# Performance work log

Hardware: AMD Instinct MI355X
Metric: run time of the kernel (lower is better)

The kernel has to match this reference:

```python
import jax, jax.numpy as jnp
import numpy as np

H = 16      # num_heads
HD = 128    # head_dim = embed_dim // num_heads
BS = 64     # NSA block_size
SEL = 8     # selected blocks per query (block_counts)
WIN = 64    # sliding window (left) size
BASE = 10000.0


def _rope(t):
    # t: [b, n, h, hd]; rotary LRPE (lrpe_type=1)
    n, hd = t.shape[1], t.shape[-1]
    half = hd // 2
    inv = 1.0 / (BASE ** (jnp.arange(half, dtype=jnp.float32) / half))
    th = jnp.arange(n, dtype=jnp.float32)[:, None] * inv[None, :]  # [n, half]
    cos = jnp.cos(th)[None, :, None, :]
    sin = jnp.sin(th)[None, :, None, :]
    t1, t2 = t[..., :half], t[..., half:]
    return jnp.concatenate([t1 * cos - t2 * sin, t1 * sin + t2 * cos], axis=-1)


def _nsa_forward(x, Wq, Wk, Wv, Wg, Wo):
    b, n, d = x.shape
    nb = n // BS
    scale = HD ** -0.5
    q = (x @ Wq).reshape(b, n, H, HD)
    k = (x @ Wk).reshape(b, n, H, HD)
    v = (x @ Wv).reshape(b, n, H, HD)
    g = jax.nn.sigmoid(x @ Wg)                   # [b, n, 3H]
    g_cmp, g_slc, g_swa = jnp.split(g, 3, axis=-1)
    q = _rope(q)
    k = _rope(k)
    idx = jnp.arange(n)

    # --- compression branch: mean-pooled KV blocks, causal over fully-past blocks
    k_cmp = k.reshape(b, nb, BS, H, HD).mean(axis=2)   # [b, nb, h, hd]
    v_cmp = v.reshape(b, nb, BS, H, HD).mean(axis=2)
    s_cmp = jnp.einsum('bnhd,bmhd->bhnm', q, k_cmp) * scale  # [b, h, n, nb]
    blk_end = (jnp.arange(nb) + 1) * BS - 1
    cmp_mask = idx[:, None] >= blk_end[None, :]        # [n, nb]
    p_cmp = jax.nn.softmax(jnp.where(cmp_mask[None, None], s_cmp, -1e30), axis=-1)
    p_cmp = p_cmp * cmp_mask.any(-1)[None, None, :, None]  # zero rows with no valid block
    o_cmp = jnp.einsum('bhnm,bmhd->bnhd', p_cmp, v_cmp)

    # --- selection branch: top-k blocks by compressed scores, current block forced
    cur_blk = jax.nn.one_hot(idx // BS, nb, dtype=jnp.float32)  # [n, nb]
    imp = p_cmp + 2.0 * cur_blk[None, None]
    sel = jax.lax.top_k(imp, SEL)[1]                   # [b, h, n, SEL]
    blk_sel = jax.nn.one_hot(sel, nb).sum(-2) > 0      # [b, h, n, nb]
    causal = idx[:, None] >= idx[None, :]              # [n, n]
    slc_mask = blk_sel[..., idx // BS] & causal[None, None]  # [b, h, n, n]
    s_full = jnp.einsum('bnhd,bmhd->bhnm', q, k) * scale     # [b, h, n, n]
    p_slc = jax.nn.softmax(jnp.where(slc_mask, s_full, -1e30), axis=-1)
    o_slc = jnp.einsum('bhnm,bmhd->bnhd', p_slc, v)

    swa_mask = causal & (idx[:, None] - idx[None, :] <= WIN)
    p_swa = jax.nn.softmax(jnp.where(swa_mask[None, None], s_full, -1e30), axis=-1)
    o_swa = jnp.einsum('bhnm,bmhd->bnhd', p_swa, v)

    o = (o_cmp * g_cmp[..., None] + o_slc * g_slc[..., None]
         + o_swa * g_swa[..., None])                   # [b, n, h, hd]
    return o.reshape(b, n, H * HD) @ Wo


def setup_inputs() -> dict:
    key = jax.random.key(0)
    ks = jax.random.split(key, 6)
    B, N, D = 2, 1024, 2048
    std = 0.02
    return {
        'x': jax.random.normal(ks[0], (B, N, D), jnp.float32),
        'Wq': jax.random.normal(ks[1], (D, H * HD), jnp.float32) * std,
        'Wk': jax.random.normal(ks[2], (D, H * HD), jnp.float32) * std,
        'Wv': jax.random.normal(ks[3], (D, H * HD), jnp.float32) * std,
        'Wg': jax.random.normal(ks[4], (D, 3 * H), jnp.float32) * std,
        'Wo': jax.random.normal(ks[5], (H * HD, D), jnp.float32) * std,
    }


def reference(x, Wq, Wk, Wv, Wg, Wo):
    return _nsa_forward(x, Wq, Wk, Wv, Wg, Wo)
```

## Files before the change

kernel.cpp:

```cpp
#include <hip/hip_runtime.h>
#include <hip/hip_bf16.h>

#define HN   16
#define HDIM 128
#define NSEQ 1024
#define NBLK 16
#define BSZ  64
#define SCALE 0.08838834764831845f
#define QKV_STR 6400
#define KOFS 2048
#define VOFS 4096
#define GOFS 6144

typedef __attribute__((ext_vector_type(8))) short bfrag;
typedef __attribute__((ext_vector_type(4))) float facc;

__device__ __forceinline__ float bf2f(short s) {
  union { unsigned u; float f; } cv;
  cv.u = ((unsigned)(unsigned short)s) << 16;
  return cv.f;
}
__device__ __forceinline__ short f2bf(float f) {
  unsigned u = __float_as_uint(f);
  u = (u + 0x7fff + ((u >> 16) & 1)) >> 16;
  return (short)u;
}

#define ASYNC16(gp, lp)                                                    \
  __builtin_amdgcn_global_load_lds(                                        \
      (const __attribute__((address_space(1))) void*)(gp),                 \
      (__attribute__((address_space(3))) void*)(lp), 16, 0, 0)

#define MFMA16(a, b, c) __builtin_amdgcn_mfma_f32_16x16x32_bf16(a, b, c, 0, 0, 0)

__global__ __launch_bounds__(256) void prep(const float* __restrict__ Wq,
                                            const float* __restrict__ Wk,
                                            const float* __restrict__ Wv,
                                            const float* __restrict__ Wg,
                                            const float* __restrict__ Wo,
                                            const float* __restrict__ x,
                                            short* __restrict__ w_t,
                                            short* __restrict__ wo_t,
                                            short* __restrict__ x_bf,
                                            float2* __restrict__ tbl) {
  __shared__ float tile[32][33];
  const int z = blockIdx.z;
  const int bx = blockIdx.x * 32, by = blockIdx.y * 32;
  const int tx = threadIdx.x & 31, ty = threadIdx.x >> 5;
  if (z == 5) {
    if (blockIdx.y >= 4) return;
    int i = (blockIdx.y * 64 + blockIdx.x) * 256 + threadIdx.x;
    int d = i & 63, n = i >> 6;
    float inv = expf(-(float)d * (9.210340371976184f / 64.0f));
    float sn, cs;
    sincosf((float)n * inv, &sn, &cs);
    tbl[i] = make_float2(cs, sn);
    return;
  }
  if (z == 4) {
#pragma unroll
    for (int i = 0; i < 4; ++i) {
      const int row = by + ty + 8 * i;
      x_bf[(size_t)row * 2048 + bx + tx] = f2bf(x[(size_t)row * 2048 + bx + tx]);
    }
    return;
  }
  if (z == 3) {
    if (blockIdx.x >= 4) return;
#pragma unroll
    for (int i = 0; i < 4; ++i) {
      const int c = bx + tx;
      tile[ty + 8 * i][tx] = (c < 48) ? Wg[(size_t)(by + ty + 8 * i) * 48 + c] : 0.f;
    }
    __syncthreads();
#pragma unroll
    for (int i = 0; i < 4; ++i)
      w_t[(size_t)(GOFS + bx + ty + 8 * i) * 2048 + by + tx] = f2bf(tile[tx][ty + 8 * i]);
    return;
  }
  if (z == 6) {
#pragma unroll
    for (int i = 0; i < 4; ++i)
      tile[ty + 8 * i][tx] = Wo[(size_t)(by + ty + 8 * i) * 2048 + bx + tx];
    __syncthreads();
#pragma unroll
    for (int i = 0; i < 4; ++i)
      wo_t[(size_t)(bx + ty + 8 * i) * 2048 + by + tx] = f2bf(tile[tx][ty + 8 * i]);
    return;
  }
  const float* src = (z == 0) ? Wq : (z == 1) ? Wk : Wv;
#pragma unroll
  for (int i = 0; i < 4; ++i)
    tile[ty + 8 * i][tx] = src[(size_t)(by + ty + 8 * i) * 2048 + bx + tx];
  __syncthreads();
#pragma unroll
  for (int i = 0; i < 4; ++i)
    w_t[(size_t)(z * 2048 + bx + ty + 8 * i) * 2048 + by + tx] = f2bf(tile[tx][ty + 8 * i]);
}

__global__ __launch_bounds__(512, 1) void gemm256(const short* __restrict__ A,
                                                  const short* __restrict__ Bt,
                                                  short* __restrict__ C,
                                                  int M, int N, int K) {
  __shared__ short lds[2][2][16384];
  const int t = threadIdx.x;
  const int l = t & 63, w = t >> 6;
  const int wm = w >> 2, wn = w & 3;
  const int lm = l & 15, hi = l >> 4;
  const int lanexor = (lm & 7) << 3;
  const int kk0 = (hi * 8) ^ lanexor;
  const int L = blockIdx.x;
  const int item = (L & 7) * (gridDim.x >> 3) + (L >> 3);
  const int nrow = M >> 8;
  const int row0 = (item % nrow) * 256, col0 = (item / nrow) * 256;
  const int nt = K >> 6;
  const int ni = nt >> 1;

  const int srow = t >> 3;
  const int scol = 8 * ((t & 7) ^ (srow & 7));
  const short* Ab = A + (size_t)(row0 + srow) * K + scol;
  const short* Bb = Bt + (size_t)(col0 + srow) * K + scol;

#define STAGE(mat, srcbase, h, tau, buf)                                     \
  {                                                                          \
    const short* g_ = (srcbase) + (size_t)(h) * 128 * K + (size_t)(tau) * 64;\
    short* d_ = &lds[buf][mat][(h) * 8192 + t * 8];                          \
    ASYNC16(g_, d_);                                                         \
    ASYNC16(g_ + (size_t)64 * K, d_ + 4096);                                 \
  }

#define DS_A(qm, cb)                                                         \
  _Pragma("unroll") for (int ii = 0; ii < 4; ++ii) {                         \
    const int row_ = wm * 128 + (qm) * 64 + ii * 16 + lm;                    \
    af[ii * 2 + 0] = *(const bfrag*)&lds[cb][0][row_ * 64 + kk0];            \
    af[ii * 2 + 1] = *(const bfrag*)&lds[cb][0][row_ * 64 + (kk0 ^ 32)];     \
  }
#define DS_B(qn, arr, cb)                                                    \
  _Pragma("unroll") for (int jj = 0; jj < 2; ++jj) {                         \
    const int row_ = wn * 64 + (qn) * 32 + jj * 16 + lm;                     \
    arr[jj * 2 + 0] = *(const bfrag*)&lds[cb][1][row_ * 64 + kk0];           \
    arr[jj * 2 + 1] = *(const bfrag*)&lds[cb][1][row_ * 64 + (kk0 ^ 32)];    \
  }
#define QUAD(qm, qn, arr)                                                    \
  _Pragma("unroll") for (int ii = 0; ii < 4; ++ii)                           \
  _Pragma("unroll") for (int jj = 0; jj < 2; ++jj) {                         \
    acc[(qm)*4+ii][(qn)*2+jj] = MFMA16(af[ii*2+0], arr[jj*2+0], acc[(qm)*4+ii][(qn)*2+jj]); \
    acc[(qm)*4+ii][(qn)*2+jj] = MFMA16(af[ii*2+1], arr[jj*2+1], acc[(qm)*4+ii][(qn)*2+jj]); \
  }
#define BARLG                                                                \
  __builtin_amdgcn_s_barrier();                                              \
  asm volatile("s_waitcnt lgkmcnt(0)" ::: "memory");                         \
  __builtin_amdgcn_sched_barrier(0)
#define PRIO1 __builtin_amdgcn_s_setprio(1)
#define PRIO0 __builtin_amdgcn_s_setprio(0)
#define BAR __builtin_amdgcn_s_barrier()

  facc acc[8][4] = {};
  bfrag af[8], bf0[4], bf1[4];

  STAGE(0, Ab, 0, 0, 0); STAGE(0, Ab, 1, 0, 0);
  STAGE(1, Bb, 0, 0, 0); STAGE(1, Bb, 1, 0, 0);
  STAGE(1, Bb, 0, 1, 1); STAGE(1, Bb, 1, 1, 1);
  asm volatile("s_waitcnt vmcnt(4)" ::: "memory");
  BAR;

  for (int i = 0; i < ni; ++i) {
    const int t1 = 2 * i + 1;
    const int g2 = (2 * i + 2 < nt) ? 2 * i + 2 : 2 * i;
    const int g3 = (2 * i + 3 < nt) ? 2 * i + 3 : t1;

    DS_A(0, 0); DS_B(0, bf0, 0);
    STAGE(0, Ab, 0, t1, 1);
    BARLG; PRIO1; QUAD(0, 0, bf0); PRIO0; BAR;

    DS_B(1, bf1, 0);
    STAGE(0, Ab, 1, t1, 1);
    BARLG; PRIO1; QUAD(0, 1, bf1); PRIO0; BAR;

    DS_A(1, 0);
    STAGE(1, Bb, 0, g2, 0);
    BARLG; PRIO1; QUAD(1, 1, bf1); PRIO0; BAR;

    STAGE(1, Bb, 1, g2, 0);
    PRIO1; QUAD(1, 0, bf0); PRIO0;
    asm volatile("s_waitcnt vmcnt(4)" ::: "memory");
    BAR;

    DS_A(0, 1); DS_B(0, bf0, 1);
    STAGE(0, Ab, 0, g2, 0);
    BARLG; PRIO1; QUAD(0, 0, bf0); PRIO0; BAR;

    DS_B(1, bf1, 1);
    STAGE(0, Ab, 1, g2, 0);
    BARLG; PRIO1; QUAD(0, 1, bf1); PRIO0; BAR;

    DS_A(1, 1);
    STAGE(1, Bb, 0, g3, 1);
    BARLG; PRIO1; QUAD(1, 1, bf1); PRIO0; BAR;

    STAGE(1, Bb, 1, g3, 1);
    PRIO1; QUAD(1, 0, bf0); PRIO0;
    asm volatile("s_waitcnt vmcnt(4)" ::: "memory");
    BAR;
  }

#pragma unroll
  for (int i = 0; i < 8; ++i)
#pragma unroll
    for (int j = 0; j < 4; ++j)
#pragma unroll
      for (int rr = 0; rr < 4; ++rr)
        C[(size_t)(row0 + wm * 128 + i * 16 + hi * 4 + rr) * N +
          col0 + wn * 64 + j * 16 + lm] = f2bf(acc[i][j][rr]);
#undef STAGE
#undef DS_A
#undef DS_B
#undef QUAD
#undef BARLG
#undef PRIO1
#undef PRIO0
#undef BAR
}

__device__ __forceinline__ void store_c(float* p, float v) { *p = v; }
__device__ __forceinline__ void store_c(short* p, float v) { *p = f2bf(v); }

template <typename OT>
__global__ __launch_bounds__(512, 1) void gemm_bf16_bt(const short* __restrict__ A,
                                                       const short* __restrict__ Bt,
                                                       OT* __restrict__ C,
                                                       int M, int N, int K) {
  __shared__ short As[128 * 32];
  __shared__ short Bs[128 * 32];
  const int t = threadIdx.x;
  const int l = t & 63, w = t >> 6;
  const int wr = w >> 2, wc = w & 3;
  const int lm = l & 15, lk = (l >> 4) * 8;
  const int L = blockIdx.x;
  const int xcd = L & 7, j = L >> 3;
  const int rowt = (xcd & 3) * 4 + (j & 3);
  const int colt = (xcd >> 2) * 8 + (j >> 2);
  const int row0 = rowt * 128, col0 = colt * 128;
  facc acc[4][2] = {};

  const int sr = t >> 2;
  const int sk = (t & 3) * 8;
  const short* Ag = A + (size_t)(row0 + sr) * K + sk;
  const short* Bg = Bt + (size_t)(col0 + sr) * K + sk;
  short* la = As + t * 8;
  short* lb = Bs + t * 8;

  for (int k0 = 0; k0 < K; k0 += 32) {
    ASYNC16(Ag + k0, la);
    ASYNC16(Bg + k0, lb);
    __syncthreads();
    bfrag af[4], bf[2];
#pragma unroll
    for (int i = 0; i < 4; ++i)
      af[i] = *(const bfrag*)&As[(wr * 64 + i * 16 + lm) * 32 + lk];
#pragma unroll
    for (int j2 = 0; j2 < 2; ++j2)
      bf[j2] = *(const bfrag*)&Bs[(wc * 32 + j2 * 16 + lm) * 32 + lk];
#pragma unroll
    for (int i = 0; i < 4; ++i)
#pragma unroll
      for (int j2 = 0; j2 < 2; ++j2)
        acc[i][j2] = MFMA16(af[i], bf[j2], acc[i][j2]);
    __syncthreads();
  }

  const int orow = row0 + wr * 64 + (l >> 4) * 4;
  const int ocol = col0 + wc * 32 + lm;
#pragma unroll
  for (int i = 0; i < 4; ++i)
#pragma unroll
    for (int j2 = 0; j2 < 2; ++j2)
#pragma unroll
      for (int rr = 0; rr < 4; ++rr)
        store_c(&C[(size_t)(orow + i * 16 + rr) * N + ocol + j2 * 16], acc[i][j2][rr]);
}

__global__ __launch_bounds__(256) void postqkv(short* __restrict__ qkv,
                                               const float2* __restrict__ tbl,
                                               float* __restrict__ kc,
                                               short* __restrict__ vt,
                                               short* __restrict__ vct) {
  const int nb = blockIdx.x, h = blockIdx.y, b = blockIdx.z;
  const int t = threadIdx.x;
  const int n0 = nb * 64;
  __shared__ short tile[64][136];

  const int row = t >> 2;
  const int c16 = (t & 3) * 16;
  const float2* tp = tbl + (size_t)(n0 + row) * 64 + c16;

#pragma unroll
  for (int qk = 0; qk < 2; ++qk) {
    short* base = qkv + (size_t)(b * NSEQ + n0 + row) * QKV_STR + qk * KOFS + h * HDIM + c16;
    bfrag lo0 = *(const bfrag*)base;
    bfrag lo1 = *(const bfrag*)(base + 8);
    bfrag hi0 = *(const bfrag*)(base + 64);
    bfrag hi1 = *(const bfrag*)(base + 72);
    bfrag olo0, olo1, ohi0, ohi1;
#pragma unroll
    for (int j = 0; j < 8; ++j) {
      float2 cs0 = tp[j], cs1 = tp[j + 8];
      float a0 = bf2f(lo0[j]), b0 = bf2f(hi0[j]);
      float a1 = bf2f(lo1[j]), b1 = bf2f(hi1[j]);
      olo0[j] = f2bf(a0 * cs0.x - b0 * cs0.y);
      ohi0[j] = f2bf(a0 * cs0.y + b0 * cs0.x);
      olo1[j] = f2bf(a1 * cs1.x - b1 * cs1.y);
      ohi1[j] = f2bf(a1 * cs1.y + b1 * cs1.x);
    }
    *(bfrag*)base = olo0;
    *(bfrag*)(base + 8) = olo1;
    *(bfrag*)(base + 64) = ohi0;
    *(bfrag*)(base + 72) = ohi1;
    if (qk == 1) {
      *(bfrag*)&tile[row][c16] = olo0;
      *(bfrag*)&tile[row][c16 + 8] = olo1;
      *(bfrag*)&tile[row][c16 + 64] = ohi0;
      *(bfrag*)&tile[row][c16 + 72] = ohi1;
    }
  }
  __syncthreads();

  if (t < 128) {
    float s = 0.f;
#pragma unroll 8
    for (int r = 0; r < 64; ++r) s += bf2f(tile[r][t]);
    kc[(((size_t)(b * NBLK + nb) * HN) + h) * 128 + t] = s * (1.0f / 64.0f);
  }
  __syncthreads();

#pragma unroll
  for (int it = 0; it < 4; ++it) {
    int idx = t + 256 * it;
    int r2 = idx >> 4, ch = idx & 15;
    *(bfrag*)&tile[r2][ch * 8] =
        *(const bfrag*)&qkv[(size_t)(b * NSEQ + n0 + r2) * QKV_STR + VOFS + h * HDIM + ch * 8];
  }
  __syncthreads();

#pragma unroll
  for (int it = 0; it < 4; ++it) {
    int idx = t + 256 * it;
    int d = idx >> 3, ch = idx & 7;
    bfrag tv;
    float s = 0.f;
#pragma unroll
    for (int j = 0; j < 8; ++j) {
      tv[j] = tile[ch * 8 + j][d];
      s += bf2f(tv[j]);
    }
    *(bfrag*)&vt[(((size_t)(b * HN + h) * 128) + d) * 1024 + n0 + ch * 8] = tv;
    s += __shfl_down(s, 4);
    s += __shfl_down(s, 2);
    s += __shfl_down(s, 1);
    if ((t & 7) == 0)
      vct[(((size_t)(b * HN + h) * 128) + d) * 16 + nb] = f2bf(s * (1.0f / 64.0f));
  }
}

__global__ __launch_bounds__(64) void cmp_sel(const short* __restrict__ qkv,
                                              const float* __restrict__ kc,
                                              short* __restrict__ pc,
                                              int* __restrict__ sel) {
  int i = blockIdx.x * 64 + threadIdx.x;
  int n = i & 1023;
  int h = (i >> 10) & 15;
  int b = i >> 14;
  const short* qp = qkv + (size_t)(b * NSEQ + n) * QKV_STR + h * HDIM;
  const int nv = (n + 1) >> 6;
  float s[NBLK];
#pragma unroll
  for (int m = 0; m < NBLK; ++m) s[m] = 0.f;
  for (int d0 = 0; d0 < HDIM; d0 += 8) {
    bfrag qv = *(const bfrag*)&qp[d0];
    float qf[8];
#pragma unroll
    for (int dd = 0; dd < 8; ++dd) qf[dd] = bf2f(qv[dd]);
    for (int m = 0; m < nv; ++m) {
      const float4* kp = (const float4*)(kc + ((size_t)((b * NBLK + m) * HN + h) << 7) + d0);
      const float4 k0 = kp[0], k1 = kp[1];
      s[m] += qf[0] * k0.x + qf[1] * k0.y + qf[2] * k0.z + qf[3] * k0.w +
              qf[4] * k1.x + qf[5] * k1.y + qf[6] * k1.z + qf[7] * k1.w;
    }
  }
  float mx = -1e30f;
  for (int m = 0; m < nv; ++m) { s[m] *= SCALE; mx = fmaxf(mx, s[m]); }
  float den = 0.f;
  for (int m = 0; m < nv; ++m) { s[m] = __expf(s[m] - mx); den += s[m]; }
  const float rden = (nv > 0) ? 1.0f / den : 0.f;
  float p[NBLK];
#pragma unroll
  for (int m = 0; m < NBLK; ++m) p[m] = (m < nv) ? s[m] * rden : 0.f;
  bfrag o0, o1;
#pragma unroll
  for (int m = 0; m < 8; ++m) { o0[m] = f2bf(p[m]); o1[m] = f2bf(p[m + 8]); }
  bfrag* pout = (bfrag*)(pc + (size_t)i * 16);
  pout[0] = o0; pout[1] = o1;
  p[n >> 6] += 2.0f;
  int mask = 0;
#pragma unroll
  for (int ss = 0; ss < 8; ++ss) {
    int best = 0;
    float bv = -1e30f;
#pragma unroll
    for (int m = 0; m < NBLK; ++m)
      if (p[m] > bv) { bv = p[m]; best = m; }
    mask |= 1 << best;
    p[best] = -1e30f;
  }
  sel[i] = mask;
}

__global__ __launch_bounds__(512, 1) void attn_mfma(
    const short* __restrict__ qkv, const short* __restrict__ vt,
    const short* __restrict__ vct, const short* __restrict__ pc,
    const int* __restrict__ sel, short* __restrict__ o) {
  const int fid = blockIdx.x;
  const int xcd = fid & 7;
  const int idx = fid >> 3;
  const int pair = (xcd << 2) | (idx & 3);
  const int rblk = idx >> 2;
  const int h = pair & 15, b = pair >> 4;

  const int tid = threadIdx.x;
  const int wid = tid >> 6;
  const int l = tid & 63;
  const int lm = l & 15, hi = l >> 4;
  const int rt = wid * 8 + rblk;
  const int nbase = rt * 16;
  const int CTMAX = ((56 + rblk) * 16) >> 6;

  __shared__ short kbuf[3][8192];
  __shared__ short vbuf[3][8192];
  __shared__ short pbuf[8][2][1024];
  short* p_slc = &pbuf[wid][0][0];
  short* p_swa = &pbuf[wid][1][0];

  const short* qrow = qkv + (size_t)(b * NSEQ + nbase + lm) * QKV_STR + h * HDIM;
  bfrag qf[4];
#pragma unroll
  for (int ks = 0; ks < 4; ++ks) qf[ks] = *(const bfrag*)&qrow[32 * ks + 8 * hi];

  int selrow = sel[(size_t)(b * HN + h) * NSEQ + nbase + lm];
  int uni = selrow;
#pragma unroll
  for (int m = 1; m < 16; m <<= 1) uni |= __shfl_xor(uni, m);
  int sel4[4];
#pragma unroll
  for (int rg = 0; rg < 4; ++rg) sel4[rg] = __shfl(selrow, 4 * hi + rg);

  const int thi = nbase >> 6;
  const int tlo = (nbase >= 64) ? ((nbase - 64) >> 6) : 0;
  const int wmask = (int)((2u << thi) - (1u << tlo));
  const unsigned am = (unsigned)(uni | wmask) & (unsigned)((2u << thi) - 1);

  facc acc_slc[8] = {}, acc_swa[8] = {};
  float ps_s[4] = {0.f, 0.f, 0.f, 0.f}, ps_w[4] = {0.f, 0.f, 0.f, 0.f};

#define STAGEKV(ct_, buf_)                                                   \
  {                                                                          \
    _Pragma("unroll") for (int rr = 0; rr < 2; ++rr) {                       \
      const int i2 = tid + 512 * rr;                                         \
      const int rw = i2 >> 4, cc = i2 & 15;                                  \
      const short* g_ = qkv + (size_t)(b * NSEQ + (ct_) * 64 + rw) * QKV_STR \
                        + KOFS + h * HDIM + 8 * (cc ^ (rw & 7));             \
      ASYNC16(g_, &kbuf[buf_][i2 * 8]);                                      \
    }                                                                        \
    _Pragma("unroll") for (int rr = 0; rr < 2; ++rr) {                       \
      const int i2 = tid + 512 * rr;                                         \
      const int dd = i2 >> 3, cc = i2 & 7;                                   \
      const short* g_ = vt + ((size_t)(b * HN + h) * 128 + dd) * 1024        \
                        + (ct_) * 64 + 8 * (cc ^ (dd & 7));                  \
      ASYNC16(g_, &vbuf[buf_][i2 * 8]);                                      \
    }                                                                        \
  }

#define EXPF(f_)                                                            \
  _Pragma("unroll") for (int rg = 0; rg < 4; ++rg) {                        \
    const int col_ = ct * 64 + 16 * (f_) + lm;                              \
    const int row_ = nbase + 4 * hi + rg;                                   \
    float e_ = __expf(sacc[f_][rg] * SCALE);                                \
    e_ = (col_ <= row_) ? e_ : 0.f;                                         \
    float es_ = ((sel4[rg] >> ct) & 1) ? e_ : 0.f;                          \
    float ew_ = (row_ - col_ <= 64) ? e_ : 0.f;                             \
    ps_s[rg] += es_;                                                        \
    ps_w[rg] += ew_;                                                        \
    const int srow_ = 4 * hi + rg;                                          \
    const int sidx_ = (64 * srow_ + 16 * (f_) + lm) ^ ((srow_ & 7) << 3);   \
    if (do_s) p_slc[sidx_] = f2bf(es_);                                     \
    if (do_w) p_swa[sidx_] = f2bf(ew_);                                     \
  }

  STAGEKV(0, 0);
  STAGEKV(1, 1);
  asm volatile("s_waitcnt vmcnt(4)" ::: "memory");
  __syncthreads();

  int cur = 0;
  for (int ct = 0; ct <= CTMAX; ++ct) {
    const bool have_next2 = (ct + 2 <= CTMAX);
    if (have_next2) {
      const int nb2 = (cur + 2 >= 3) ? cur - 1 : cur + 2;
      const int ct2 = ct + 2;
      STAGEKV(ct2, nb2);
    }

    if ((am >> ct) & 1) {
      const bool do_s = (uni >> ct) & 1;
      const bool do_w = (wmask >> ct) & 1;

      facc sacc[4] = {};
#pragma unroll
      for (int f = 0; f < 4; ++f) {
        const int row_ = 16 * f + lm;
        const int rx = row_ & 7;
        bfrag k0 = *(const bfrag*)&kbuf[cur][row_ * 128 + 8 * ((0 + hi) ^ rx)];
        bfrag k1 = *(const bfrag*)&kbuf[cur][row_ * 128 + 8 * ((4 + hi) ^ rx)];
        bfrag k2 = *(const bfrag*)&kbuf[cur][row_ * 128 + 8 * ((8 + hi) ^ rx)];
        bfrag k3 = *(const bfrag*)&kbuf[cur][row_ * 128 + 8 * ((12 + hi) ^ rx)];
        sacc[f] = MFMA16(qf[0], k0, sacc[f]);
        sacc[f] = MFMA16(qf[1], k1, sacc[f]);
        sacc[f] = MFMA16(qf[2], k2, sacc[f]);
        sacc[f] = MFMA16(qf[3], k3, sacc[f]);
      }

      EXPF(0); EXPF(1); EXPF(2); EXPF(3);

#pragma unroll
      for (int ks = 0; ks < 2; ++ks) {
        const int ridx = (64 * lm + 8 * hi + 32 * ks) ^ ((lm & 7) << 3);
        bfrag pas = {}, paw = {};
        if (do_s) pas = *(const bfrag*)&p_slc[ridx];
        if (do_w) paw = *(const bfrag*)&p_swa[ridx];
#pragma unroll
        for (int df = 0; df < 8; ++df) {
          const int d_ = 16 * df + lm;
          bfrag vb = *(const bfrag*)&vbuf[cur][d_ * 64 + 8 * ((4 * ks + hi) ^ (d_ & 7))];
          if (do_s) acc_slc[df] = MFMA16(pas, vb, acc_slc[df]);
          if (do_w) acc_swa[df] = MFMA16(paw, vb, acc_swa[df]);
        }
      }
    }

    if (ct < CTMAX) {
      if (have_next2)
        asm volatile("s_waitcnt vmcnt(4)" ::: "memory");
      else
        asm volatile("s_waitcnt vmcnt(0)" ::: "memory");
      __syncthreads();
    }
    cur = (cur + 1 >= 3) ? 0 : cur + 1;
  }
#undef STAGEKV
#undef EXPF

  facc acc_cmp[8] = {};
  {
    bfrag pa = {};
    if (hi < 2)
      pa = *(const bfrag*)&pc[((size_t)(b * HN + h) * NSEQ + nbase + lm) * 16 + 8 * hi];
#pragma unroll
    for (int df = 0; df < 8; ++df) {
      bfrag vb = {};
      if (hi < 2)
        vb = *(const bfrag*)&vct[(((size_t)(b * HN + h) * 128) + 16 * df + lm) * 16 + 8 * hi];
      acc_cmp[df] = MFMA16(pa, vb, acc_cmp[df]);
    }
  }

#pragma unroll
  for (int m = 1; m < 16; m <<= 1) {
#pragma unroll
    for (int rg = 0; rg < 4; ++rg) {
      ps_s[rg] += __shfl_xor(ps_s[rg], m);
      ps_w[rg] += __shfl_xor(ps_w[rg], m);
    }
  }

  float inv_s[4], inv_w[4], gcv[4], gsv[4], gwv[4];
#pragma unroll
  for (int rg = 0; rg < 4; ++rg) {
    inv_s[rg] = 1.0f / ps_s[rg];
    inv_w[rg] = 1.0f / ps_w[rg];
    const short* gp = qkv + (size_t)(b * NSEQ + nbase + 4 * hi + rg) * QKV_STR + GOFS;
    gcv[rg] = 1.0f / (1.0f + __expf(-bf2f(gp[h])));
    gsv[rg] = 1.0f / (1.0f + __expf(-bf2f(gp[16 + h])));
    gwv[rg] = 1.0f / (1.0f + __expf(-bf2f(gp[32 + h])));
  }

  short* obase = o + (size_t)(b * NSEQ + nbase) * 2048 + h * HDIM;
#pragma unroll
  for (int df = 0; df < 8; ++df)
#pragma unroll
    for (int rg = 0; rg < 4; ++rg) {
      float val = gcv[rg] * acc_cmp[df][rg] +
                  gsv[rg] * acc_slc[df][rg] * inv_s[rg] +
                  gwv[rg] * acc_swa[df][rg] * inv_w[rg];
      obase[(size_t)(4 * hi + rg) * 2048 + 16 * df + lm] = f2bf(val);
    }
}

extern "C" void kernel_launch(void* const* d_in, const int* in_sizes, int n_in,
                              void* d_out, int out_size, void* d_ws, size_t ws_size,
                              hipStream_t stream) {
  const float* x  = (const float*)d_in[0];
  const float* Wq = (const float*)d_in[1];
  const float* Wk = (const float*)d_in[2];
  const float* Wv = (const float*)d_in[3];
  const float* Wg = (const float*)d_in[4];
  const float* Wo = (const float*)d_in[5];
  float* out = (float*)d_out;

  char* w = (char*)d_ws;
  short* x_bf = (short*)w;
  short* o_bf = x_bf;
  w += (size_t)2048 * 2048 * 2;
  short* w_t  = (short*)w;
  w += (size_t)6400 * 2048 * 2;
  short* qkv  = (short*)w;
  w += (size_t)2048 * 6400 * 2;
  float* kc   = (float*)w; w += (size_t)65536 * 4;
  short* vct  = (short*)w; w += (size_t)65536 * 2;
  short* pcb  = (short*)w; w += (size_t)524288 * 2;
  int*   sel  = (int*)w;   w += (size_t)32768 * 4;
  short* vt   = (short*)w; w += (size_t)4194304 * 2;
  float2* tbl = (float2*)w; w += (size_t)65536 * 8;
  short* wo_t = (short*)w; w += (size_t)2048 * 2048 * 2;

  const dim3 blk(256);
  prep<<<dim3(64, 64, 7), blk, 0, stream>>>(Wq, Wk, Wv, Wg, Wo, x, w_t, wo_t, x_bf, tbl);
  gemm256<<<200, dim3(512), 0, stream>>>(x_bf, w_t, qkv, 2048, 6400, 2048);
  postqkv<<<dim3(16, 16, 2), blk, 0, stream>>>(qkv, tbl, kc, vt, vct);
  cmp_sel<<<512, dim3(64), 0, stream>>>(qkv, kc, pcb, sel);
  attn_mfma<<<256, dim3(512), 0, stream>>>(qkv, vt, vct, pcb, sel, o_bf);
  gemm_bf16_bt<float><<<256, dim3(512), 0, stream>>>(o_bf, wo_t, out, 2048, 2048, 2048);
}
```

Baseline: 226.5 us.

## Replace 256x256 QKV GEMM with 128x128 tiled kernel over 800 blocks

The fused QKV+gate projection GEMM moves from a 256x256 tile with 512 threads and a 4-phase double-buffered schedule to a 128x128 tile with 256 threads and a simpler per-k-step double buffer. The grid grows from 200 to 800 workgroups, which fills the device's compute units more evenly instead of leaving some idle with 200 large tiles. In exchange, per-tile data reuse is halved, so more global and LDS traffic is needed, and the pipeline waits on vmcnt(0) every step, which exposes load latency.

```diff
diff --git a/kernel.cpp b/kernel.cpp
--- a/kernel.cpp
+++ b/kernel.cpp
@@ -98,128 +98,100 @@
     w_t[(size_t)(z * 2048 + bx + ty + 8 * i) * 2048 + by + tx] = f2bf(tile[tx][ty + 8 * i]);
 }
 
-__global__ __launch_bounds__(512, 1) void gemm256(const short* __restrict__ A,
+__global__ __launch_bounds__(256, 1) void gemm128(const short* __restrict__ A,
                                                   const short* __restrict__ Bt,
                                                   short* __restrict__ C,
                                                   int M, int N, int K) {
-  __shared__ short lds[2][2][16384];
+  __shared__ short lds[2][2][8192];
   const int t = threadIdx.x;
   const int l = t & 63, w = t >> 6;
-  const int wm = w >> 2, wn = w & 3;
+  const int wr = w >> 1, wc = w & 1;
   const int lm = l & 15, hi = l >> 4;
-  const int lanexor = (lm & 7) << 3;
-  const int kk0 = (hi * 8) ^ lanexor;
+  const int r7 = lm & 7;
+  const int kk0 = 8 * (hi ^ r7);
   const int L = blockIdx.x;
   const int item = (L & 7) * (gridDim.x >> 3) + (L >> 3);
-  const int nrow = M >> 8;
-  const int row0 = (item % nrow) * 256, col0 = (item / nrow) * 256;
+  const int nrow = M >> 7;
+  const int row0 = (item % nrow) * 128, col0 = (item / nrow) * 128;
   const int nt = K >> 6;
-  const int ni = nt >> 1;
-
-  const int srow = t >> 3;
-  const int scol = 8 * ((t & 7) ^ (srow & 7));
-  const short* Ab = A + (size_t)(row0 + srow) * K + scol;
-  const short* Bb = Bt + (size_t)(col0 + srow) * K + scol;
-
-#define STAGE(mat, srcbase, h, tau, buf)                                     \
-  {                                                                          \
-    const short* g_ = (srcbase) + (size_t)(h) * 128 * K + (size_t)(tau) * 64;\
-    short* d_ = &lds[buf][mat][(h) * 8192 + t * 8];                          \
-    ASYNC16(g_, d_);                                                         \
-    ASYNC16(g_ + (size_t)64 * K, d_ + 4096);                                 \
-  }
-
-#define DS_A(qm, cb)                                                         \
+
+  const short* Ab = A + (size_t)row0 * K;
+  const short* Bb = Bt + (size_t)col0 * K;
+
+#define STG(mat, base, tau, buf)                                             \
+  _Pragma("unroll") for (int j2 = 0; j2 < 4; ++j2) {                         \
+    const int idx2 = t + 256 * j2;                                           \
+    const int rw = idx2 >> 3, cc = idx2 & 7;                                 \
+    ASYNC16((base) + (size_t)rw * K + (size_t)(tau) * 64 + 8 * (cc ^ (rw & 7)), \
+            &lds[buf][mat][idx2 * 8]);                                       \
+  }
+#define DS_A(cb)                                                             \
   _Pragma("unroll") for (int ii = 0; ii < 4; ++ii) {                         \
-    const int row_ = wm * 128 + (qm) * 64 + ii * 16 + lm;                    \
+    const int row_ = wr * 64 + ii * 16 + lm;                                 \
     af[ii * 2 + 0] = *(const bfrag*)&lds[cb][0][row_ * 64 + kk0];            \
     af[ii * 2 + 1] = *(const bfrag*)&lds[cb][0][row_ * 64 + (kk0 ^ 32)];     \
   }
-#define DS_B(qn, arr, cb)                                                    \
+#define DS_B(q, arr, cb)                                                     \
   _Pragma("unroll") for (int jj = 0; jj < 2; ++jj) {                         \
-    const int row_ = wn * 64 + (qn) * 32 + jj * 16 + lm;                     \
+    const int row_ = wc * 64 + (q) * 32 + jj * 16 + lm;                      \
     arr[jj * 2 + 0] = *(const bfrag*)&lds[cb][1][row_ * 64 + kk0];           \
     arr[jj * 2 + 1] = *(const bfrag*)&lds[cb][1][row_ * 64 + (kk0 ^ 32)];    \
   }
-#define QUAD(qm, qn, arr)                                                    \
+#define HALF(q, arr)                                                         \
   _Pragma("unroll") for (int ii = 0; ii < 4; ++ii)                           \
   _Pragma("unroll") for (int jj = 0; jj < 2; ++jj) {                         \
-    acc[(qm)*4+ii][(qn)*2+jj] = MFMA16(af[ii*2+0], arr[jj*2+0], acc[(qm)*4+ii][(qn)*2+jj]); \
-    acc[(qm)*4+ii][(qn)*2+jj] = MFMA16(af[ii*2+1], arr[jj*2+1], acc[(qm)*4+ii][(qn)*2+jj]); \
+    acc[ii][(q)*2+jj] = MFMA16(af[ii*2+0], arr[jj*2+0], acc[ii][(q)*2+jj]);  \
+    acc[ii][(q)*2+jj] = MFMA16(af[ii*2+1], arr[jj*2+1], acc[ii][(q)*2+jj]);  \
   }
 #define BARLG                                                                \
   __builtin_amdgcn_s_barrier();                                              \
   asm volatile("s_waitcnt lgkmcnt(0)" ::: "memory");                         \
   __builtin_amdgcn_sched_barrier(0)
-#define PRIO1 __builtin_amdgcn_s_setprio(1)
-#define PRIO0 __builtin_amdgcn_s_setprio(0)
-#define BAR __builtin_amdgcn_s_barrier()
-
-  facc acc[8][4] = {};
+
+  facc acc[4][4] = {};
   bfrag af[8], bf0[4], bf1[4];
 
-  STAGE(0, Ab, 0, 0, 0); STAGE(0, Ab, 1, 0, 0);
-  STAGE(1, Bb, 0, 0, 0); STAGE(1, Bb, 1, 0, 0);
-  STAGE(1, Bb, 0, 1, 1); STAGE(1, Bb, 1, 1, 1);
-  asm volatile("s_waitcnt vmcnt(4)" ::: "memory");
-  BAR;
-
-  for (int i = 0; i < ni; ++i) {
-    const int t1 = 2 * i + 1;
-    const int g2 = (2 * i + 2 < nt) ? 2 * i + 2 : 2 * i;
-    const int g3 = (2 * i + 3 < nt) ? 2 * i + 3 : t1;
-
-    DS_A(0, 0); DS_B(0, bf0, 0);
-    STAGE(0, Ab, 0, t1, 1);
-    BARLG; PRIO1; QUAD(0, 0, bf0); PRIO0; BAR;
-
-    DS_B(1, bf1, 0);
-    STAGE(0, Ab, 1, t1, 1);
-    BARLG; PRIO1; QUAD(0, 1, bf1); PRIO0; BAR;
-
-    DS_A(1, 0);
-    STAGE(1, Bb, 0, g2, 0);
-    BARLG; PRIO1; QUAD(1, 1, bf1); PRIO0; BAR;
-
-    STAGE(1, Bb, 1, g2, 0);
-    PRIO1; QUAD(1, 0, bf0); PRIO0;
-    asm volatile("s_waitcnt vmcnt(4)" ::: "memory");
-    BAR;
-
-    DS_A(0, 1); DS_B(0, bf0, 1);
-    STAGE(0, Ab, 0, g2, 0);
-    BARLG; PRIO1; QUAD(0, 0, bf0); PRIO0; BAR;
-
-    DS_B(1, bf1, 1);
-    STAGE(0, Ab, 1, g2, 0);
-    BARLG; PRIO1; QUAD(0, 1, bf1); PRIO0; BAR;
-
-    DS_A(1, 1);
-    STAGE(1, Bb, 0, g3, 1);
-    BARLG; PRIO1; QUAD(1, 1, bf1); PRIO0; BAR;
-
-    STAGE(1, Bb, 1, g3, 1);
-    PRIO1; QUAD(1, 0, bf0); PRIO0;
-    asm volatile("s_waitcnt vmcnt(4)" ::: "memory");
-    BAR;
-  }
-
-#pragma unroll
-  for (int i = 0; i < 8; ++i)
+  STG(0, Ab, 0, 0);
+  STG(1, Bb, 0, 0);
+  asm volatile("s_waitcnt vmcnt(0)" ::: "memory");
+  __builtin_amdgcn_s_barrier();
+
+  for (int tau = 0; tau < nt; ++tau) {
+    const int c = tau & 1;
+    const int tn = (tau + 1 < nt) ? tau + 1 : tau;
+
+    DS_A(c); DS_B(0, bf0, c);
+    STG(0, Ab, tn, c ^ 1);
+    BARLG;
+    __builtin_amdgcn_s_setprio(1);
+    HALF(0, bf0);
+    __builtin_amdgcn_s_setprio(0);
+    __builtin_amdgcn_s_barrier();
+
+    DS_B(1, bf1, c);
+    STG(1, Bb, tn, c ^ 1);
+    BARLG;
+    __builtin_amdgcn_s_setprio(1);
+    HALF(1, bf1);
+    __builtin_amdgcn_s_setprio(0);
+    asm volatile("s_waitcnt vmcnt(0)" ::: "memory");
+    __builtin_amdgcn_s_barrier();
+  }
+
+  const int orow = row0 + wr * 64 + hi * 4;
+  const int ocol = col0 + wc * 64 + lm;
+#pragma unroll
+  for (int i = 0; i < 4; ++i)
 #pragma unroll
     for (int j = 0; j < 4; ++j)
 #pragma unroll
       for (int rr = 0; rr < 4; ++rr)
-        C[(size_t)(row0 + wm * 128 + i * 16 + hi * 4 + rr) * N +
-          col0 + wn * 64 + j * 16 + lm] = f2bf(acc[i][j][rr]);
-#undef STAGE
+        C[(size_t)(orow + i * 16 + rr) * N + ocol + j * 16] = f2bf(acc[i][j][rr]);
+#undef STG
 #undef DS_A
 #undef DS_B
-#undef QUAD
+#undef HALF
 #undef BARLG
-#undef PRIO1
-#undef PRIO0
-#undef BAR
 }
 
 __device__ __forceinline__ void store_c(float* p, float v) { *p = v; }
@@ -633,7 +605,7 @@
 
   const dim3 blk(256);
   prep<<<dim3(64, 64, 7), blk, 0, stream>>>(Wq, Wk, Wv, Wg, Wo, x, w_t, wo_t, x_bf, tbl);
-  gemm256<<<200, dim3(512), 0, stream>>>(x_bf, w_t, qkv, 2048, 6400, 2048);
+  gemm128<<<800, blk, 0, stream>>>(x_bf, w_t, qkv, 2048, 6400, 2048);
   postqkv<<<dim3(16, 16, 2), blk, 0, stream>>>(qkv, tbl, kc, vt, vct);
   cmp_sel<<<512, dim3(64), 0, stream>>>(qkv, kc, pcb, sel);
   attn_mfma<<<256, dim3(512), 0, stream>>>(qkv, vt, vct, pcb, sel, o_bf);
```

After: 237.1 us. +4.7%, slower.
